# Optimization experiments

Hardware: AMD Instinct MI355X
Metric: run time of the kernel (lower is better)

Reference implementation:

```python
import jax, jax.numpy as jnp
import numpy as np

B, LQ, LK = 8, 2048, 2048
HIST_DIM, COMB_DIM, FUSION_DIM = 1024, 1024, 1024


def _linear_params(key, in_dim, out_dim):
    k1, k2 = jax.random.split(key)
    bound = 1.0 / np.sqrt(in_dim)
    W = jax.random.uniform(k1, (out_dim, in_dim), jnp.float32, -bound, bound)
    b = jax.random.uniform(k2, (out_dim,), jnp.float32, -bound, bound)
    return W, b


def setup_inputs() -> dict:
    key = jax.random.key(0)
    ks = jax.random.split(key, 8)
    hW, hb = _linear_params(ks[0], HIST_DIM, FUSION_DIM)
    cW, cb = _linear_params(ks[1], COMB_DIM, FUSION_DIM)
    qW, qb = _linear_params(ks[2], FUSION_DIM, FUSION_DIM)
    kW, kb = _linear_params(ks[3], FUSION_DIM, FUSION_DIM)
    vW, vb = _linear_params(ks[4], FUSION_DIM, FUSION_DIM)
    oW, ob = _linear_params(ks[5], FUSION_DIM, FUSION_DIM)
    return {
        "history_features": jax.random.normal(ks[6], (B, LQ, HIST_DIM), jnp.float32),
        "combined_features": jax.random.normal(ks[7], (B, LK, COMB_DIM), jnp.float32),
        "hW": hW, "hb": hb, "cW": cW, "cb": cb,
        "qW": qW, "qb": qb, "kW": kW, "kb": kb,
        "vW": vW, "vb": vb, "oW": oW, "ob": ob,
    }


def _lin(x, W, b):
    # torch nn.Linear: y = x @ W.T + b
    return jnp.einsum('bld,fd->blf', x, W) + b


def reference(history_features, combined_features, hW, hb, cW, cb, qW, qb, kW, kb, vW, vb, oW, ob):
    h = _lin(history_features, hW, hb)      # [B, LQ, F]
    c = _lin(combined_features, cW, cb)     # [B, LK, F]
    q = _lin(h, qW, qb)
    k = _lin(c, kW, kb)
    v = _lin(c, vW, vb)
    scale = 1.0 / jnp.sqrt(jnp.float32(FUSION_DIM))
    scores = jnp.einsum('bqf,bkf->bqk', q, k) * scale
    attn = jax.nn.softmax(scores, axis=-1)
    attn_out = jnp.einsum('bqk,bkf->bqf', attn, v)
    return _lin(attn_out + q, oW, ob)
```

## Files before the change

kernel.cpp:

```cpp
#include <hip/hip_runtime.h>
#include <stdint.h>

using bf16x8 = __attribute__((ext_vector_type(8))) short;
using f32x4  = __attribute__((ext_vector_type(4))) float;
using u16x4  = __attribute__((ext_vector_type(4))) unsigned short;
using u16x8  = __attribute__((ext_vector_type(8))) unsigned short;

__device__ __forceinline__ unsigned short f2bf(float f) {
  unsigned u = __builtin_bit_cast(unsigned, f);
  u = (u + 0x7FFFu + ((u >> 16) & 1u)) >> 16;
  return (unsigned short)u;
}
__device__ __forceinline__ float bf2f(unsigned short h) {
  unsigned u = ((unsigned)h) << 16;
  return __builtin_bit_cast(float, u);
}

__global__ __launch_bounds__(256) void cvt_f32_to_bf16(
    const float* __restrict__ in, unsigned short* __restrict__ out, long n8) {
  long i = (long)blockIdx.x * blockDim.x + threadIdx.x;
  const long stride = (long)gridDim.x * blockDim.x;
  for (; i < n8; i += stride) {
    float4 a = ((const float4*)in)[2 * i];
    float4 b = ((const float4*)in)[2 * i + 1];
    u16x8 o = { f2bf(a.x), f2bf(a.y), f2bf(a.z), f2bf(a.w),
                f2bf(b.x), f2bf(b.y), f2bf(b.z), f2bf(b.w) };
    ((u16x8*)out)[i] = o;
  }
}

__global__ __launch_bounds__(256) void transpose_cast(
    const float* __restrict__ in, unsigned short* __restrict__ out, int R, int C) {
  __shared__ unsigned short tile[64][68];
  const int c0 = blockIdx.x * 64, r0 = blockIdx.y * 64;
  const int t = threadIdx.x;
#pragma unroll
  for (int i = 0; i < 4; ++i) {
    int ch = t + i * 256;
    int r = ch >> 4, c4 = (ch & 15) * 4;
    float4 v = *(const float4*)&in[(size_t)(r0 + r) * C + c0 + c4];
    u16x4 o = { f2bf(v.x), f2bf(v.y), f2bf(v.z), f2bf(v.w) };
    *(u16x4*)&tile[r][c4] = o;
  }
  __syncthreads();
#pragma unroll
  for (int i = 0; i < 4; ++i) {
    int ch = t + i * 256;
    int r = ch >> 4, c4 = (ch & 15) * 4;
    u16x4 v;
#pragma unroll
    for (int j = 0; j < 4; ++j) v[j] = tile[c4 + j][r];
    *(u16x4*)&out[(size_t)(c0 + r) * R + r0 + c4] = v;
  }
}

__global__ __launch_bounds__(256) void bias_matvec(
    const float* __restrict__ W, const float* __restrict__ x,
    const float* __restrict__ b, float* __restrict__ out, int n) {
  const int row = blockIdx.x;
  const float* wr = W + (long)row * n;
  float s = 0.f;
  for (int j = threadIdx.x; j < n; j += 256) s += wr[j] * x[j];
#pragma unroll
  for (int o = 32; o; o >>= 1) s += __shfl_xor(s, o);
  __shared__ float red[4];
  if ((threadIdx.x & 63) == 0) red[threadIdx.x >> 6] = s;
  __syncthreads();
  if (threadIdx.x == 0) out[row] = red[0] + red[1] + red[2] + red[3] + b[row];
}

__global__ __launch_bounds__(256) void softmax_rows_bf16(
    unsigned short* __restrict__ S, int ncol) {
  const long row = blockIdx.x;
  unsigned short* rp = S + row * (long)ncol;
  const int t = threadIdx.x;
  u16x8 raw = *(const u16x8*)&rp[t * 8];
  float v[8];
  float mx = -3.0e38f;
#pragma unroll
  for (int j = 0; j < 8; ++j) { v[j] = bf2f(raw[j]); mx = fmaxf(mx, v[j]); }
#pragma unroll
  for (int o = 32; o; o >>= 1) mx = fmaxf(mx, __shfl_xor(mx, o));
  __shared__ float redm[4], reds[4];
  if ((t & 63) == 0) redm[t >> 6] = mx;
  __syncthreads();
  mx = fmaxf(fmaxf(redm[0], redm[1]), fmaxf(redm[2], redm[3]));
  float s = 0.f;
#pragma unroll
  for (int j = 0; j < 8; ++j) { v[j] = __expf(v[j] - mx); s += v[j]; }
#pragma unroll
  for (int o = 32; o; o >>= 1) s += __shfl_xor(s, o);
  if ((t & 63) == 0) reds[t >> 6] = s;
  __syncthreads();
  const float inv = 1.f / (reds[0] + reds[1] + reds[2] + reds[3]);
  u16x8 o8;
#pragma unroll
  for (int j = 0; j < 8; ++j) o8[j] = f2bf(v[j] * inv);
  *(u16x8*)&rp[t * 8] = o8;
}

template <int EPI>
__global__ __launch_bounds__(256, 4) void gemm_bt(
    const unsigned short* __restrict__ A, const unsigned short* __restrict__ B,
    void* __restrict__ C, const float* __restrict__ bias,
    const unsigned short* __restrict__ resid,
    int M, int N, int K, long sA, long sB, long sC, long sR, float scale) {
  __shared__ unsigned short lA[2][128][32];
  __shared__ unsigned short lB[2][128][32];
  const int t = threadIdx.x;
  const int gx = gridDim.x, gy = gridDim.y;
  int bid = blockIdx.x + gx * (blockIdx.y + gy * blockIdx.z);
  const int nwg = gx * gy * (int)gridDim.z;
  const int chunk = nwg >> 3;
  int lid = (bid & 7) * chunk + (bid >> 3);
  const int bn = lid % gx; lid /= gx;
  const int bm = lid % gy;
  const int bz = lid / gy;

  const unsigned short* Ab = A + (long)bz * sA + (long)bm * 128 * K;
  const unsigned short* Bb = B + (long)bz * sB + (long)bn * 128 * K;

  const int lane = t & 63;
  const int wv = t >> 6, wm = wv >> 1, wn = wv & 1;
  const int fr = lane & 15, kg = lane >> 4;
  const int srow  = t >> 2;
  const int scol  = (t & 3) * 8;
  const int wbyte = (t >> 6) * 1024;

  f32x4 acc[4][4] = {};
  const int NT = K >> 5;

  auto stage = [&](int buf, int kt) {
    const unsigned short* sa = Ab + kt * 32;
    const unsigned short* sb = Bb + kt * 32;
#pragma unroll
    for (int p = 0; p < 2; ++p) {
      const unsigned short* srcA = sa + (long)(p * 64 + srow) * K + scol;
      const unsigned short* srcB = sb + (long)(p * 64 + srow) * K + scol;
      char* dA = (char*)(&lA[buf][0][0]) + p * 4096 + wbyte;
      char* dB = (char*)(&lB[buf][0][0]) + p * 4096 + wbyte;
      __builtin_amdgcn_global_load_lds(
          (const __attribute__((address_space(1))) void*)srcA,
          (__attribute__((address_space(3))) void*)dA, 16, 0, 0);
      __builtin_amdgcn_global_load_lds(
          (const __attribute__((address_space(1))) void*)srcB,
          (__attribute__((address_space(3))) void*)dB, 16, 0, 0);
    }
  };

  stage(0, 0);
  for (int kt = 0; kt < NT; ++kt) {
    const int cur = kt & 1;
    __syncthreads();
    if (kt + 1 < NT) stage(cur ^ 1, kt + 1);
    bf16x8 av[4], bv[4];
#pragma unroll
    for (int m = 0; m < 4; ++m)
      av[m] = *(const bf16x8*)&lA[cur][wm * 64 + m * 16 + fr][kg * 8];
#pragma unroll
    for (int n = 0; n < 4; ++n)
      bv[n] = *(const bf16x8*)&lB[cur][wn * 64 + n * 16 + fr][kg * 8];
#pragma unroll
    for (int m = 0; m < 4; ++m)
#pragma unroll
      for (int n = 0; n < 4; ++n)
        acc[m][n] = __builtin_amdgcn_mfma_f32_16x16x32_bf16(av[m], bv[n], acc[m][n], 0, 0, 0);
  }

  const int row0 = bm * 128 + wm * 64 + kg * 4;
  const int col0 = bn * 128 + wn * 64 + fr;
  const long cb = (long)bz * sC;
#pragma unroll
  for (int m = 0; m < 4; ++m)
#pragma unroll
    for (int n = 0; n < 4; ++n) {
      const int col = col0 + n * 16;
#pragma unroll
      for (int r = 0; r < 4; ++r) {
        const int row = row0 + m * 16 + r;
        float v = acc[m][n][r];
        if constexpr (EPI == 1) {
          v *= scale;
          ((unsigned short*)C)[cb + (long)row * N + col] = f2bf(v);
        } else {
          v += bias[col];
          ((unsigned short*)C)[cb + (long)row * N + col] = f2bf(v);
        }
      }
    }
}

template <int EPI>
__global__ __launch_bounds__(512, 2) void gemm256(
    const unsigned short* __restrict__ A, const unsigned short* __restrict__ B,
    void* __restrict__ C, const float* __restrict__ bias,
    const unsigned short* __restrict__ resid,
    int N, int K, long sA, long sB, long sC, long sR, float scale) {
  __shared__ char lds[131072];
  const int t = threadIdx.x;
  const int lane = t & 63, wid = t >> 6;

  const int gx = gridDim.x, gy = gridDim.y;
  int bid = blockIdx.x + gx * (blockIdx.y + gy * blockIdx.z);
  const int nwg = gx * gy * (int)gridDim.z;
  const int chunk = nwg >> 3;
  int lid = (bid & 7) * chunk + (bid >> 3);
  const int bn = lid % gx; lid /= gx;
  const int bm = lid % gy;
  const int bz = lid / gy;

  const unsigned short* Ab = A + (long)bz * sA + (long)bm * 256 * K;
  const unsigned short* Bb = B + (long)bz * sB + (long)bn * 256 * K;

  const int colswz = ((lane & 3) * 8) ^ ((lane >> 5) * 16);
  const int r0s = (wid >> 1) * 16 + (lane >> 2);
  const int scol = (wid & 1) * 32 + colswz;

  const int wm = wid >> 2, wn = wid & 3;
  const int fr = lane & 15, kg = lane >> 4;
  const int lanePart = (fr * 64 + kg * 16) ^ ((fr >> 3) << 5);

  auto issue = [&](const unsigned short* base, int kt, int h, int bufbyte) {
#pragma unroll
    for (int s = 0; s < 2; ++s) {
      const unsigned short* src = base + (long)(h * 128 + r0s + s * 64) * K + kt * 64 + scol;
      char* dst = lds + bufbyte + h * 16384 + s * 8192 + wid * 1024;
      __builtin_amdgcn_global_load_lds(
          (const __attribute__((address_space(1))) void*)src,
          (__attribute__((address_space(3))) void*)dst, 16, 0, 0);
    }
  };

  f32x4 acc[8][4] = {};
  const int NT = K >> 6;
  const int NITER = NT >> 1;

  issue(Ab, 0, 0, 0);      issue(Ab, 0, 1, 0);
  issue(Bb, 0, 0, 65536);  issue(Bb, 0, 1, 65536);
  issue(Bb, 1, 0, 98304);  issue(Bb, 1, 1, 98304);
  asm volatile("s_waitcnt vmcnt(4)" ::: "memory");
  __builtin_amdgcn_s_barrier();

  for (int it = 0; it < NITER; ++it) {
    const int kt0 = it * 2;
    const bool last = (it == NITER - 1);
#pragma unroll
    for (int hf = 0; hf < 2; ++hf) {
      const int abuf = hf * 32768;
      const int bbuf = 65536 + hf * 32768;
      bf16x8 bv[4][2];
      bf16x8 av[2][2];
#pragma unroll
      for (int mp = 0; mp < 4; ++mp) {
        if (mp == 0) {
#pragma unroll
          for (int n = 0; n < 4; ++n)
#pragma unroll
            for (int kk = 0; kk < 2; ++kk)
              bv[n][kk] = *(const bf16x8*)(lds + bbuf + ((wn * 4 + n) * 2 + kk) * 1024 + lanePart);
        }
#pragma unroll
        for (int ml = 0; ml < 2; ++ml)
#pragma unroll
          for (int kk = 0; kk < 2; ++kk)
            av[ml][kk] = *(const bf16x8*)(lds + abuf + ((wm * 8 + mp * 2 + ml) * 2 + kk) * 1024 + lanePart);
        if (hf == 0) {
          if (mp == 0) issue(Ab, kt0 + 1, 0, 32768);
          else if (mp == 1) { issue(Ab, kt0 + 1, 1, 32768); if (!last) issue(Bb, kt0 + 2, 0, 65536); }
          else if (mp == 2) { if (!last) issue(Bb, kt0 + 2, 1, 65536); }
          else {
            if (last) asm volatile("s_waitcnt vmcnt(0)" ::: "memory");
            else      asm volatile("s_waitcnt vmcnt(4)" ::: "memory");
          }
        } else if (!last) {
          if (mp == 0) issue(Ab, kt0 + 2, 0, 0);
          else if (mp == 1) { issue(Ab, kt0 + 2, 1, 0); issue(Bb, kt0 + 3, 0, 98304); }
          else if (mp == 2) issue(Bb, kt0 + 3, 1, 98304);
          else asm volatile("s_waitcnt vmcnt(4)" ::: "memory");
        }
        __builtin_amdgcn_s_barrier();
        __builtin_amdgcn_s_setprio(1);
#pragma unroll
        for (int kk = 0; kk < 2; ++kk)
#pragma unroll
          for (int ml = 0; ml < 2; ++ml)
#pragma unroll
            for (int n = 0; n < 4; ++n)
              acc[mp * 2 + ml][n] = __builtin_amdgcn_mfma_f32_16x16x32_bf16(
                  av[ml][kk], bv[n][kk], acc[mp * 2 + ml][n], 0, 0, 0);
        __builtin_amdgcn_s_setprio(0);
        asm volatile("s_waitcnt lgkmcnt(0)" ::: "memory");
        __builtin_amdgcn_s_barrier();
      }
    }
  }

  const int row0 = bm * 256 + wm * 128 + kg * 4;
  const int col0 = bn * 256 + wn * 64 + fr;
  const long cb = (long)bz * sC;
#pragma unroll
  for (int m = 0; m < 8; ++m)
#pragma unroll
    for (int n = 0; n < 4; ++n) {
      const int col = col0 + n * 16;
#pragma unroll
      for (int r = 0; r < 4; ++r) {
        const int row = row0 + m * 16 + r;
        float v = acc[m][n][r];
        if constexpr (EPI == 0) {
          v += bias[col];
          ((unsigned short*)C)[cb + (long)row * N + col] = f2bf(v);
        } else if constexpr (EPI == 1) {
          v *= scale;
          ((unsigned short*)C)[cb + (long)row * N + col] = f2bf(v);
        } else if constexpr (EPI == 2) {
          v += bf2f(resid[(long)bz * sR + (long)row * N + col]);
          ((unsigned short*)C)[cb + (long)row * N + col] = f2bf(v);
        } else if constexpr (EPI == 3) {
          v += bias[col];
          ((float*)C)[cb + (long)row * N + col] = v;
        } else {
          v += bias[row];
          ((unsigned short*)C)[cb + (long)row * N + col] = f2bf(v);
        }
      }
    }
}

extern "C" void kernel_launch(void* const* d_in, const int* in_sizes, int n_in,
                              void* d_out, int out_size, void* d_ws, size_t ws_size,
                              hipStream_t stream) {
  (void)in_sizes; (void)n_in; (void)out_size; (void)ws_size;
  const float* hist = (const float*)d_in[0];
  const float* comb = (const float*)d_in[1];
  const float* hW = (const float*)d_in[2];  const float* hb = (const float*)d_in[3];
  const float* cW = (const float*)d_in[4];  const float* cb = (const float*)d_in[5];
  const float* qW = (const float*)d_in[6];  const float* qb = (const float*)d_in[7];
  const float* kW = (const float*)d_in[8];  const float* kb = (const float*)d_in[9];
  const float* vW = (const float*)d_in[10]; const float* vb = (const float*)d_in[11];
  const float* oW = (const float*)d_in[12]; const float* ob = (const float*)d_in[13];

  constexpr int  Bn = 8, L = 2048, F = 1024;
  constexpr long NE = (long)Bn * L * F;
  constexpr long WE = (long)F * F;

  char* ws = (char*)d_ws;
  size_t off = 0;
  unsigned short* oWb = (unsigned short*)(ws + off); off += WE * 2;
  unsigned short* Wq  = (unsigned short*)(ws + off); off += WE * 2;
  unsigned short* Wkv = (unsigned short*)(ws + off); off += 2 * WE * 2;
  unsigned short* Wk  = Wkv;
  unsigned short* Wv  = Wkv + WE;
  float* bq = (float*)(ws + off); off += F * 4;
  float* bk = (float*)(ws + off); off += F * 4;
  float* bv = (float*)(ws + off); off += F * 4;
  unsigned short* A0 = (unsigned short*)(ws + off); off += NE * 2;
  unsigned short* A1 = (unsigned short*)(ws + off); off += NE * 2;
  unsigned short* A2 = (unsigned short*)(ws + off); off += NE * 2;
  unsigned short* A3 = (unsigned short*)(ws + off); off += NE * 2;
  unsigned short* S  = (unsigned short*)(ws + off); off += (size_t)Bn * L * L * 2;
  unsigned short* hWt = S;
  unsigned short* cWt = S + WE;
  unsigned short* qWb = S + 2 * WE;
  unsigned short* kvWb = S + 3 * WE;

  transpose_cast<<<dim3(16, 16, 1), 256, 0, stream>>>(hW, hWt, F, F);
  transpose_cast<<<dim3(16, 16, 1), 256, 0, stream>>>(cW, cWt, F, F);
  cvt_f32_to_bf16<<<512, 256, 0, stream>>>(qW, qWb, WE / 8);
  cvt_f32_to_bf16<<<512, 256, 0, stream>>>(kW, kvWb, WE / 8);
  cvt_f32_to_bf16<<<512, 256, 0, stream>>>(vW, kvWb + WE, WE / 8);
  cvt_f32_to_bf16<<<512, 256, 0, stream>>>(oW, oWb, WE / 8);
  cvt_f32_to_bf16<<<2048, 256, 0, stream>>>(hist, A0, NE / 8);
  cvt_f32_to_bf16<<<2048, 256, 0, stream>>>(comb, A1, NE / 8);

  bias_matvec<<<F, 256, 0, stream>>>(qW, hb, qb, bq, F);
  bias_matvec<<<F, 256, 0, stream>>>(kW, cb, kb, bk, F);
  bias_matvec<<<F, 256, 0, stream>>>(vW, cb, vb, bv, F);

  gemm_bt<1><<<dim3(8, 8, 1), 256, 0, stream>>>(qWb, hWt, Wq, nullptr, nullptr,
      1024, 1024, 1024, 0, 0, 0, 0, 1.0f);
  gemm_bt<1><<<dim3(8, 16, 1), 256, 0, stream>>>(kvWb, cWt, Wkv, nullptr, nullptr,
      2048, 1024, 1024, 0, 0, 0, 0, 1.0f);

  const float SCALE = 0.03125f;

  gemm256<0><<<dim3(4, 64, 1), 512, 0, stream>>>(A0, Wq, A2, bq, nullptr,
      1024, 1024, 0, 0, 0, 0, 0.f);
  gemm256<0><<<dim3(4, 64, 1), 512, 0, stream>>>(A1, Wk, A0, bk, nullptr,
      1024, 1024, 0, 0, 0, 0, 0.f);
  gemm256<4><<<dim3(8, 4, Bn), 512, 0, stream>>>(Wv, A1, A3, bv, nullptr,
      2048, 1024, 0, (long)L * F, (long)F * L, 0, 0.f);
  gemm256<1><<<dim3(8, 8, Bn), 512, 0, stream>>>(A2, A0, S, nullptr, nullptr,
      2048, 1024, (long)L * F, (long)L * F, (long)L * L, 0, SCALE);
  softmax_rows_bf16<<<Bn * L, 256, 0, stream>>>(S, L);
  gemm256<2><<<dim3(4, 8, Bn), 512, 0, stream>>>(S, A3, A1, nullptr, A2,
      1024, 2048, (long)L * L, (long)F * L, (long)L * F, (long)L * F, 0.f);
  gemm256<3><<<dim3(4, 64, 1), 512, 0, stream>>>(A1, oWb, (float*)d_out, ob, nullptr,
      1024, 1024, 0, 0, 0, 0, 0.f);
}
```

Measured before the change: 413.2 us.

## Fuse softmax exp into QK GEMM epilogue and defer normalization to PV GEMM

Removes the separate softmax pass over the score matrix. The QK^T GEMM epilogue now writes exp2 of the scaled scores together with per-tile row-sum partials, a tiny kernel merges those into inverse row sums, and the PV GEMM epilogue applies the normalization and the residual add. It also drops the key bias, since it only adds a per-row constant to the scores, and removes one barrier per inner loop step in the main GEMM. The risks are that no max is subtracted before exponentiation, so large scores could overflow, and that the barrier reordering could create an LDS race.

```diff
diff --git a/kernel.cpp b/kernel.cpp
--- a/kernel.cpp
+++ b/kernel.cpp
@@ -69,56 +69,36 @@
   if (threadIdx.x == 0) out[row] = red[0] + red[1] + red[2] + red[3] + b[row];
 }
 
-__global__ __launch_bounds__(256) void softmax_rows_bf16(
-    unsigned short* __restrict__ S, int ncol) {
-  const long row = blockIdx.x;
-  unsigned short* rp = S + row * (long)ncol;
-  const int t = threadIdx.x;
-  u16x8 raw = *(const u16x8*)&rp[t * 8];
-  float v[8];
-  float mx = -3.0e38f;
-#pragma unroll
-  for (int j = 0; j < 8; ++j) { v[j] = bf2f(raw[j]); mx = fmaxf(mx, v[j]); }
-#pragma unroll
-  for (int o = 32; o; o >>= 1) mx = fmaxf(mx, __shfl_xor(mx, o));
-  __shared__ float redm[4], reds[4];
-  if ((t & 63) == 0) redm[t >> 6] = mx;
-  __syncthreads();
-  mx = fmaxf(fmaxf(redm[0], redm[1]), fmaxf(redm[2], redm[3]));
-  float s = 0.f;
-#pragma unroll
-  for (int j = 0; j < 8; ++j) { v[j] = __expf(v[j] - mx); s += v[j]; }
-#pragma unroll
-  for (int o = 32; o; o >>= 1) s += __shfl_xor(s, o);
-  if ((t & 63) == 0) reds[t >> 6] = s;
-  __syncthreads();
-  const float inv = 1.f / (reds[0] + reds[1] + reds[2] + reds[3]);
-  u16x8 o8;
-#pragma unroll
-  for (int j = 0; j < 8; ++j) o8[j] = f2bf(v[j] * inv);
-  *(u16x8*)&rp[t * 8] = o8;
+__global__ __launch_bounds__(256) void merge_invl(
+    const float* __restrict__ Lpart, float* __restrict__ invL, long nrows) {
+  long r = (long)blockIdx.x * 256 + threadIdx.x;
+  if (r < nrows) {
+    const float* p = Lpart + r * 8;
+    float s = 0.f;
+#pragma unroll
+    for (int i = 0; i < 8; ++i) s += p[i];
+    invL[r] = 1.f / s;
+  }
 }
 
 template <int EPI>
 __global__ __launch_bounds__(256, 4) void gemm_bt(
     const unsigned short* __restrict__ A, const unsigned short* __restrict__ B,
     void* __restrict__ C, const float* __restrict__ bias,
-    const unsigned short* __restrict__ resid,
-    int M, int N, int K, long sA, long sB, long sC, long sR, float scale) {
+    int M, int N, int K, float scale) {
   __shared__ unsigned short lA[2][128][32];
   __shared__ unsigned short lB[2][128][32];
   const int t = threadIdx.x;
   const int gx = gridDim.x, gy = gridDim.y;
-  int bid = blockIdx.x + gx * (blockIdx.y + gy * blockIdx.z);
-  const int nwg = gx * gy * (int)gridDim.z;
+  int bid = blockIdx.x + gx * blockIdx.y;
+  const int nwg = gx * gy;
   const int chunk = nwg >> 3;
   int lid = (bid & 7) * chunk + (bid >> 3);
-  const int bn = lid % gx; lid /= gx;
-  const int bm = lid % gy;
-  const int bz = lid / gy;
-
-  const unsigned short* Ab = A + (long)bz * sA + (long)bm * 128 * K;
-  const unsigned short* Bb = B + (long)bz * sB + (long)bn * 128 * K;
+  const int bn = lid % gx;
+  const int bm = lid / gx;
+
+  const unsigned short* Ab = A + (long)bm * 128 * K;
+  const unsigned short* Bb = B + (long)bn * 128 * K;
 
   const int lane = t & 63;
   const int wv = t >> 6, wm = wv >> 1, wn = wv & 1;
@@ -169,7 +149,6 @@
 
   const int row0 = bm * 128 + wm * 64 + kg * 4;
   const int col0 = bn * 128 + wn * 64 + fr;
-  const long cb = (long)bz * sC;
 #pragma unroll
   for (int m = 0; m < 4; ++m)
 #pragma unroll
@@ -179,13 +158,8 @@
       for (int r = 0; r < 4; ++r) {
         const int row = row0 + m * 16 + r;
         float v = acc[m][n][r];
-        if constexpr (EPI == 1) {
-          v *= scale;
-          ((unsigned short*)C)[cb + (long)row * N + col] = f2bf(v);
-        } else {
-          v += bias[col];
-          ((unsigned short*)C)[cb + (long)row * N + col] = f2bf(v);
-        }
+        if constexpr (EPI == 1) v *= scale; else v += bias[col];
+        ((unsigned short*)C)[(long)row * N + col] = f2bf(v);
       }
     }
 }
@@ -194,7 +168,7 @@
 __global__ __launch_bounds__(512, 2) void gemm256(
     const unsigned short* __restrict__ A, const unsigned short* __restrict__ B,
     void* __restrict__ C, const float* __restrict__ bias,
-    const unsigned short* __restrict__ resid,
+    const unsigned short* __restrict__ resid, float* __restrict__ aux,
     int N, int K, long sA, long sB, long sC, long sR, float scale) {
   __shared__ char lds[131072];
   const int t = threadIdx.x;
@@ -278,6 +252,7 @@
           else if (mp == 2) issue(Bb, kt0 + 3, 1, 98304);
           else asm volatile("s_waitcnt vmcnt(4)" ::: "memory");
         }
+        asm volatile("s_waitcnt lgkmcnt(0)" ::: "memory");
         __builtin_amdgcn_s_barrier();
         __builtin_amdgcn_s_setprio(1);
 #pragma unroll
@@ -289,8 +264,6 @@
               acc[mp * 2 + ml][n] = __builtin_amdgcn_mfma_f32_16x16x32_bf16(
                   av[ml][kk], bv[n][kk], acc[mp * 2 + ml][n], 0, 0, 0);
         __builtin_amdgcn_s_setprio(0);
-        asm volatile("s_waitcnt lgkmcnt(0)" ::: "memory");
-        __builtin_amdgcn_s_barrier();
       }
     }
   }
@@ -298,6 +271,36 @@
   const int row0 = bm * 256 + wm * 128 + kg * 4;
   const int col0 = bn * 256 + wn * 64 + fr;
   const long cb = (long)bz * sC;
+
+  if constexpr (EPI == 5) {
+    float* lf = (float*)lds;
+#pragma unroll
+    for (int m = 0; m < 8; ++m) {
+#pragma unroll
+      for (int r = 0; r < 4; ++r) {
+        const int row = row0 + m * 16 + r;
+        float sv = 0.f;
+#pragma unroll
+        for (int n = 0; n < 4; ++n) {
+          float e = exp2f(acc[m][n][r] * scale);
+          unsigned short eb = f2bf(e);
+          ((unsigned short*)C)[cb + (long)row * N + col0 + n * 16] = eb;
+          sv += bf2f(eb);
+        }
+#pragma unroll
+        for (int o = 1; o < 16; o <<= 1) sv += __shfl_xor(sv, o);
+        if ((lane & 15) == 0)
+          lf[wn * 256 + wm * 128 + m * 16 + kg * 4 + r] = sv;
+      }
+    }
+    __syncthreads();
+    if (t < 256) {
+      float s4 = lf[t] + lf[256 + t] + lf[512 + t] + lf[768 + t];
+      aux[((long)bz * 2048 + bm * 256 + t) * 8 + bn] = s4;
+    }
+    return;
+  }
+
 #pragma unroll
   for (int m = 0; m < 8; ++m)
 #pragma unroll
@@ -313,14 +316,14 @@
         } else if constexpr (EPI == 1) {
           v *= scale;
           ((unsigned short*)C)[cb + (long)row * N + col] = f2bf(v);
-        } else if constexpr (EPI == 2) {
-          v += bf2f(resid[(long)bz * sR + (long)row * N + col]);
-          ((unsigned short*)C)[cb + (long)row * N + col] = f2bf(v);
         } else if constexpr (EPI == 3) {
           v += bias[col];
           ((float*)C)[cb + (long)row * N + col] = v;
+        } else if constexpr (EPI == 4) {
+          v += bias[row];
+          ((unsigned short*)C)[cb + (long)row * N + col] = f2bf(v);
         } else {
-          v += bias[row];
+          v = v * bias[(long)bz * 2048 + row] + bf2f(resid[(long)bz * sR + (long)row * N + col]);
           ((unsigned short*)C)[cb + (long)row * N + col] = f2bf(v);
         }
       }
@@ -336,7 +339,7 @@
   const float* hW = (const float*)d_in[2];  const float* hb = (const float*)d_in[3];
   const float* cW = (const float*)d_in[4];  const float* cb = (const float*)d_in[5];
   const float* qW = (const float*)d_in[6];  const float* qb = (const float*)d_in[7];
-  const float* kW = (const float*)d_in[8];  const float* kb = (const float*)d_in[9];
+  const float* kW = (const float*)d_in[8];
   const float* vW = (const float*)d_in[10]; const float* vb = (const float*)d_in[11];
   const float* oW = (const float*)d_in[12]; const float* ob = (const float*)d_in[13];
 
@@ -352,8 +355,9 @@
   unsigned short* Wk  = Wkv;
   unsigned short* Wv  = Wkv + WE;
   float* bq = (float*)(ws + off); off += F * 4;
-  float* bk = (float*)(ws + off); off += F * 4;
   float* bv = (float*)(ws + off); off += F * 4;
+  float* Lpart = (float*)(ws + off); off += (size_t)Bn * L * 8 * 4;
+  float* invL  = (float*)(ws + off); off += (size_t)Bn * L * 4;
   unsigned short* A0 = (unsigned short*)(ws + off); off += NE * 2;
   unsigned short* A1 = (unsigned short*)(ws + off); off += NE * 2;
   unsigned short* A2 = (unsigned short*)(ws + off); off += NE * 2;
@@ -374,27 +378,26 @@
   cvt_f32_to_bf16<<<2048, 256, 0, stream>>>(comb, A1, NE / 8);
 
   bias_matvec<<<F, 256, 0, stream>>>(qW, hb, qb, bq, F);
-  bias_matvec<<<F, 256, 0, stream>>>(kW, cb, kb, bk, F);
   bias_matvec<<<F, 256, 0, stream>>>(vW, cb, vb, bv, F);
 
-  gemm_bt<1><<<dim3(8, 8, 1), 256, 0, stream>>>(qWb, hWt, Wq, nullptr, nullptr,
-      1024, 1024, 1024, 0, 0, 0, 0, 1.0f);
-  gemm_bt<1><<<dim3(8, 16, 1), 256, 0, stream>>>(kvWb, cWt, Wkv, nullptr, nullptr,
-      2048, 1024, 1024, 0, 0, 0, 0, 1.0f);
-
-  const float SCALE = 0.03125f;
-
-  gemm256<0><<<dim3(4, 64, 1), 512, 0, stream>>>(A0, Wq, A2, bq, nullptr,
+  gemm_bt<1><<<dim3(8, 8, 1), 256, 0, stream>>>(qWb, hWt, Wq, nullptr,
+      1024, 1024, 1024, 1.0f);
+  gemm_bt<1><<<dim3(8, 16, 1), 256, 0, stream>>>(kvWb, cWt, Wkv, nullptr,
+      2048, 1024, 1024, 1.0f);
+
+  const float S2 = 0.03125f * 1.44269504089f;
+
+  gemm256<0><<<dim3(4, 64, 1), 512, 0, stream>>>(A0, Wq, A2, bq, nullptr, nullptr,
       1024, 1024, 0, 0, 0, 0, 0.f);
-  gemm256<0><<<dim3(4, 64, 1), 512, 0, stream>>>(A1, Wk, A0, bk, nullptr,
+  gemm256<1><<<dim3(4, 64, 1), 512, 0, stream>>>(A1, Wk, A0, nullptr, nullptr, nullptr,
+      1024, 1024, 0, 0, 0, 0, 1.0f);
+  gemm256<4><<<dim3(8, 4, Bn), 512, 0, stream>>>(Wv, A1, A3, bv, nullptr, nullptr,
+      2048, 1024, 0, (long)L * F, (long)F * L, 0, 0.f);
+  gemm256<5><<<dim3(8, 8, Bn), 512, 0, stream>>>(A2, A0, S, nullptr, nullptr, Lpart,
+      2048, 1024, (long)L * F, (long)L * F, (long)L * L, 0, S2);
+  merge_invl<<<64, 256, 0, stream>>>(Lpart, invL, (long)Bn * L);
+  gemm256<6><<<dim3(4, 8, Bn), 512, 0, stream>>>(S, A3, A1, invL, A2, nullptr,
+      1024, 2048, (long)L * L, (long)F * L, (long)L * F, (long)L * F, 0.f);
+  gemm256<3><<<dim3(4, 64, 1), 512, 0, stream>>>(A1, oWb, (float*)d_out, ob, nullptr, nullptr,
       1024, 1024, 0, 0, 0, 0, 0.f);
-  gemm256<4><<<dim3(8, 4, Bn), 512, 0, stream>>>(Wv, A1, A3, bv, nullptr,
-      2048, 1024, 0, (long)L * F, (long)F * L, 0, 0.f);
-  gemm256<1><<<dim3(8, 8, Bn), 512, 0, stream>>>(A2, A0, S, nullptr, nullptr,
-      2048, 1024, (long)L * F, (long)L * F, (long)L * L, 0, SCALE);
-  softmax_rows_bf16<<<Bn * L, 256, 0, stream>>>(S, L);
-  gemm256<2><<<dim3(4, 8, Bn), 512, 0, stream>>>(S, A3, A1, nullptr, A2,
-      1024, 2048, (long)L * L, (long)F * L, (long)L * F, (long)L * F, 0.f);
-  gemm256<3><<<dim3(4, 64, 1), 512, 0, stream>>>(A1, oWb, (float*)d_out, ob, nullptr,
-      1024, 1024, 0, 0, 0, 0, 0.f);
-}
+}
```

Result: faster. 393.9 us (-4.7%).
